# Kernel tuning notes

Hardware: AMD Instinct MI355X
Metric: run time of the kernel (lower is better)

## Reference

```python
import jax, jax.numpy as jnp
import numpy as np

HEAD_SIZE = 64
BLOCK_SIZE = 4096
BATCH = 4


def setup_inputs() -> dict:
    key = jax.random.key(0)
    kx, kk, kq, kv = jax.random.split(key, 4)
    x = jax.random.normal(kx, (BATCH, BLOCK_SIZE, HEAD_SIZE), dtype=jnp.float32)
    s = HEAD_SIZE ** -0.5  # ~ torch default linear init scale
    Wk = jax.random.uniform(kk, (HEAD_SIZE, HEAD_SIZE), jnp.float32, -s, s)
    Wq = jax.random.uniform(kq, (HEAD_SIZE, HEAD_SIZE), jnp.float32, -s, s)
    Wv = jax.random.uniform(kv, (HEAD_SIZE, HEAD_SIZE), jnp.float32, -s, s)
    return {"x": x, "Wk": Wk, "Wq": Wq, "Wv": Wv}


def reference(x, Wk, Wq, Wv):
    # x: [B, T, C]; W*: [C, C] stored torch-style (out, in) -> y = x @ W.T
    B, T, C = x.shape
    k = x @ Wk.T  # [B, T, C]
    q = x @ Wq.T
    v = x @ Wv.T
    scores = jnp.einsum('btc,bsc->bts', q, k) * (C ** -0.5)  # [B, T, T]
    causal = jnp.tril(jnp.ones((T, T), dtype=bool))
    scores = jnp.where(causal, scores, -jnp.inf)
    weights = jax.nn.softmax(scores, axis=-1)
    out = jnp.einsum('bts,bsc->btc', weights, v)  # [B, T, C]
    return out
```

## Files before the change

kernel.cpp:

```cpp
#include <hip/hip_runtime.h>
#include <hip/hip_bf16.h>

typedef unsigned short u16;
typedef unsigned int u32;
typedef __bf16 bf16x8_t __attribute__((ext_vector_type(8)));
typedef float f32x4_t __attribute__((ext_vector_type(4)));

constexpr int Bb = 4;
constexpr int Tt = 4096;
constexpr int Dd = 64;
constexpr float QSCALE = 0.18033688011112042f;

__device__ __forceinline__ u16 f2bf(float f) {
  unsigned int u = __builtin_bit_cast(unsigned int, f);
  return (u16)((u + 0x7fffu + ((u >> 16) & 1u)) >> 16);
}
__device__ __forceinline__ u32 pk2(float a, float b) {
  return (u32)f2bf(a) | ((u32)f2bf(b) << 16);
}
__device__ __forceinline__ u32 pkt(float a, float b) {
  const u32 ua = __builtin_bit_cast(u32, a);
  const u32 ub = __builtin_bit_cast(u32, b);
  return (ua >> 16) | (ub & 0xFFFF0000u);
}
__device__ __forceinline__ bf16x8_t ld16(const u16* p) {
  int4 v = *(const int4*)p;
  return __builtin_bit_cast(bf16x8_t, v);
}
__device__ __forceinline__ bf16x8_t cvtld8(const float* p) {
  float4 a = ((const float4*)p)[0];
  float4 b = ((const float4*)p)[1];
  union { u32 u[4]; bf16x8_t v; } r;
  r.u[0] = pk2(a.x, a.y); r.u[1] = pk2(a.z, a.w);
  r.u[2] = pk2(b.x, b.y); r.u[3] = pk2(b.z, b.w);
  return r.v;
}
__device__ __forceinline__ f32x4_t mfma16(bf16x8_t a, bf16x8_t b, f32x4_t c) {
  return __builtin_amdgcn_mfma_f32_16x16x32_bf16(a, b, c, 0, 0, 0);
}

__global__ __launch_bounds__(256) void HeadV1_proj(
    const float* __restrict__ x, const float* __restrict__ Wk,
    const float* __restrict__ Wq, const float* __restrict__ Wv,
    u16* __restrict__ qS, u16* __restrict__ kS, u16* __restrict__ vS)
{
  __shared__ u16 ylds[64][72];

  const int t = threadIdx.x;
  const int w = t >> 6, lane = t & 63, l15 = lane & 15, quad = lane >> 4;
  const int r0 = blockIdx.x * 64;
  const int b  = r0 >> 12;
  const int kt = (r0 & 4095) >> 6;
  const long tilebase = ((long)(b * 64 + kt)) * 4096;

  bf16x8_t xf[2];
  #pragma unroll
  for (int kh = 0; kh < 2; kh++)
    xf[kh] = cvtld8(x + (long)(r0 + w * 16 + l15) * 64 + kh * 32 + quad * 8);

  const float* Ws[3] = {Wk, Wq, Wv};
  u16* dsts[3];
  dsts[0] = kS + tilebase; dsts[1] = qS + tilebase; dsts[2] = vS + tilebase;

  #pragma unroll
  for (int m = 0; m < 3; m++) {
    float vals[4][4];
    #pragma unroll
    for (int g = 0; g < 4; g++) {
      f32x4_t acc = {0.f, 0.f, 0.f, 0.f};
      #pragma unroll
      for (int kh = 0; kh < 2; kh++) {
        bf16x8_t wf = cvtld8(Ws[m] + (g * 16 + l15) * 64 + kh * 32 + quad * 8);
        acc = mfma16(xf[kh], wf, acc);
      }
      #pragma unroll
      for (int r = 0; r < 4; r++)
        vals[g][r] = (m == 1) ? acc[r] * QSCALE : acc[r];
    }
    #pragma unroll
    for (int g = 0; g < 4; g++)
      #pragma unroll
      for (int r = 0; r < 4; r++)
        ylds[w * 16 + quad * 4 + r][g * 16 + l15] = f2bf(vals[g][r]);
    __syncthreads();
    if (m < 2) {
      #pragma unroll
      for (int kk = 0; kk < 2; kk++) {
        bf16x8_t f = ld16(&ylds[w * 16 + l15][kk * 32 + quad * 8]);
        *(int4*)(dsts[m] + (w * 2 + kk) * 512 + lane * 8) = __builtin_bit_cast(int4, f);
      }
    } else {
      #pragma unroll
      for (int kk = 0; kk < 2; kk++) {
        u16 tmp[8];
        #pragma unroll
        for (int j = 0; j < 8; j++)
          tmp[j] = ylds[kk * 32 + quad * 8 + j][w * 16 + l15];
        *(int4*)(dsts[2] + (kk * 4 + w) * 512 + lane * 8) = *(const int4*)tmp;
      }
    }
    __syncthreads();
  }
}

__global__ __launch_bounds__(512, 2) void HeadV1_flash(
    const u16* __restrict__ qS, const u16* __restrict__ kS,
    const u16* __restrict__ vS, float* __restrict__ outg)
{
  __shared__ __align__(16) char smem[56320];
  u16  (*pT)[32][72]   = (u16 (*)[32][72])smem;
  float (*chk)[16][68] = (float (*)[16][68])smem;
  float (*stg)[68]     = (float (*)[68])(smem + 36864);
  float (*lst)[64]     = (float (*)[64])(smem + 54272);

  const int t    = threadIdx.x;
  const int w    = t >> 6;
  const int lane = t & 63;
  const int l15  = lane & 15;
  const int quad = lane >> 4;

  const int b  = blockIdx.x & 3;
  const int qt = 63 - (blockIdx.x >> 2);
  const int qr0 = qt * 64;
  const long base = (long)b * Tt * Dd;

  union { u32 u4[4]; bf16x8_t v; } uo;
  uo.u4[0] = uo.u4[1] = uo.u4[2] = uo.u4[3] = 0x3F803F80u;
  const bf16x8_t ones = uo.v;
  const f32x4_t zero4 = {0.f, 0.f, 0.f, 0.f};

  const u16* qtile = qS + ((long)(b * 64 + qt)) * 4096 + lane * 8;
  bf16x8_t qfrag[4][2];
  #pragma unroll
  for (int ct = 0; ct < 4; ct++)
    #pragma unroll
    for (int kk = 0; kk < 2; kk++)
      qfrag[ct][kk] = ld16(qtile + (ct * 2 + kk) * 512);

  f32x4_t O[4][4];
  #pragma unroll
  for (int a = 0; a < 4; a++)
    #pragma unroll
    for (int c = 0; c < 4; c++)
      O[a][c] = zero4;
  f32x4_t Lc[4] = {zero4, zero4, zero4, zero4};

  const int nk = qt + 1;

  for (int kt = w; kt < nk; kt += 8) {
    const bool ismask = (kt == qt);
    const u16* ktile = kS + ((long)(b * 64 + kt)) * 4096 + lane * 8;
    const u16* vtile = vS + ((long)(b * 64 + kt)) * 4096 + lane * 8;

    bf16x8_t kfrag[4][2];
    #pragma unroll
    for (int rt = 0; rt < 4; rt++)
      #pragma unroll
      for (int kk = 0; kk < 2; kk++)
        kfrag[rt][kk] = ld16(ktile + (rt * 2 + kk) * 512);
    bf16x8_t vf[2][4];
    #pragma unroll
    for (int kk = 0; kk < 2; kk++)
      #pragma unroll
      for (int dt = 0; dt < 4; dt++)
        vf[kk][dt] = ld16(vtile + (kk * 4 + dt) * 512);

    #pragma unroll
    for (int half = 0; half < 2; half++) {
      #pragma unroll
      for (int rt = 0; rt < 4; rt++) {
        f32x4_t acc[2];
        #pragma unroll
        for (int cl = 0; cl < 2; cl++) {
          const int ct = half * 2 + cl;
          f32x4_t a = zero4;
          a = mfma16(kfrag[rt][0], qfrag[ct][0], a);
          a = mfma16(kfrag[rt][1], qfrag[ct][1], a);
          acc[cl] = a;
        }
        if (ismask) {
          const int kvl = rt * 16 + quad * 4;
          #pragma unroll
          for (int cl = 0; cl < 2; cl++) {
            const int ql = half * 32 + cl * 16 + l15;
            #pragma unroll
            for (int r = 0; r < 4; r++)
              if (kvl + r > ql) acc[cl][r] = -1e30f;
          }
        }
        #pragma unroll
        for (int cl = 0; cl < 2; cl++) {
          const float p0 = __builtin_amdgcn_exp2f(acc[cl][0]);
          const float p1 = __builtin_amdgcn_exp2f(acc[cl][1]);
          const float p2 = __builtin_amdgcn_exp2f(acc[cl][2]);
          const float p3 = __builtin_amdgcn_exp2f(acc[cl][3]);
          uint2 pk;
          pk.x = pkt(p0, p1);
          pk.y = pkt(p2, p3);
          *(uint2*)&pT[w][cl * 16 + l15][rt * 16 + quad * 4] = pk;
        }
      }
      #pragma unroll
      for (int kk = 0; kk < 2; kk++) {
        bf16x8_t pf0 = ld16(&pT[w][l15][kk * 32 + quad * 8]);
        bf16x8_t pf1 = ld16(&pT[w][16 + l15][kk * 32 + quad * 8]);
        #pragma unroll
        for (int dt = 0; dt < 4; dt++) {
          O[dt][half * 2]     = mfma16(vf[kk][dt], pf0, O[dt][half * 2]);
          O[dt][half * 2 + 1] = mfma16(vf[kk][dt], pf1, O[dt][half * 2 + 1]);
        }
        Lc[half * 2]     = mfma16(ones, pf0, Lc[half * 2]);
        Lc[half * 2 + 1] = mfma16(ones, pf1, Lc[half * 2 + 1]);
      }
    }
  }

  if (quad == 0) {
    #pragma unroll
    for (int ct = 0; ct < 4; ct++)
      lst[w][ct * 16 + l15] = Lc[ct][0];
  }
  __syncthreads();

  #pragma unroll
  for (int dt = 0; dt < 4; dt++) {
    #pragma unroll
    for (int ct = 0; ct < 4; ct++)
      #pragma unroll
      for (int r = 0; r < 4; r++)
        chk[w][quad * 4 + r][ct * 16 + l15] = O[dt][ct][r];
    __syncthreads();
    #pragma unroll
    for (int h = 0; h < 2; h++) {
      const int pos = t + h * 512;
      const int d2 = pos >> 6, q = pos & 63;
      float s = 0.f;
      #pragma unroll
      for (int w2 = 0; w2 < 8; w2++) s += chk[w2][d2][q];
      stg[q][dt * 16 + d2] = s;
    }
    __syncthreads();
  }

  {
    const int q = t >> 3, d0 = (t & 7) * 8;
    float L = 0.f;
    #pragma unroll
    for (int w2 = 0; w2 < 8; w2++) L += lst[w2][q];
    const float invL = 1.0f / L;
    float ov[8];
    #pragma unroll
    for (int i = 0; i < 8; i++) ov[i] = stg[q][d0 + i] * invL;
    float* dst = outg + base + (long)(qr0 + q) * 64 + d0;
    *(float4*)dst       = *(const float4*)&ov[0];
    *(float4*)(dst + 4) = *(const float4*)&ov[4];
  }
}

extern "C" void kernel_launch(void* const* d_in, const int* in_sizes, int n_in,
                              void* d_out, int out_size, void* d_ws, size_t ws_size,
                              hipStream_t stream) {
  (void)in_sizes; (void)n_in; (void)out_size; (void)ws_size;
  const float* x  = (const float*)d_in[0];
  const float* Wk = (const float*)d_in[1];
  const float* Wq = (const float*)d_in[2];
  const float* Wv = (const float*)d_in[3];
  float* out = (float*)d_out;
  u16* qw  = (u16*)d_ws;
  u16* kw  = qw + (size_t)Bb * Tt * Dd;
  u16* vw  = kw + (size_t)Bb * Tt * Dd;

  HeadV1_proj<<<(Bb * Tt) / 64, 256, 0, stream>>>(x, Wk, Wq, Wv, qw, kw, vw);
  HeadV1_flash<<<256, 512, 0, stream>>>(qw, kw, vw, out);
}
```

Before: 90.53 us.

## Prefetch next K/V tile into registers and relax launch bounds occupancy

Each wave now loads the K and V fragments for its next key tile into registers while computing on the current tile, double-buffering global loads to hide memory latency. The launch bounds minimum blocks per CU drops from 2 to 1, which lets the compiler use more registers for the extra buffers. The cost is roughly double the fragment register footprint and possibly lower occupancy, which reduces latency hiding across waves. A loop variable is also renamed in the reduction epilogue.

```diff
diff --git a/kernel.cpp b/kernel.cpp
--- a/kernel.cpp
+++ b/kernel.cpp
@@ -103,7 +103,7 @@
   }
 }
 
-__global__ __launch_bounds__(512, 2) void HeadV1_flash(
+__global__ __launch_bounds__(512, 1) void HeadV1_flash(
     const u16* __restrict__ qS, const u16* __restrict__ kS,
     const u16* __restrict__ vS, float* __restrict__ outg)
 {
@@ -147,23 +147,42 @@
 
   const int nk = qt + 1;
 
+  bf16x8_t kcur[4][2], vcur[2][4];
+  if (w < nk) {
+    const u16* kt0 = kS + ((long)(b * 64 + w)) * 4096 + lane * 8;
+    const u16* vt0 = vS + ((long)(b * 64 + w)) * 4096 + lane * 8;
+    #pragma unroll
+    for (int rt = 0; rt < 4; rt++)
+      #pragma unroll
+      for (int kk = 0; kk < 2; kk++)
+        kcur[rt][kk] = ld16(kt0 + (rt * 2 + kk) * 512);
+    #pragma unroll
+    for (int kk = 0; kk < 2; kk++)
+      #pragma unroll
+      for (int dt = 0; dt < 4; dt++)
+        vcur[kk][dt] = ld16(vt0 + (kk * 4 + dt) * 512);
+  }
+
   for (int kt = w; kt < nk; kt += 8) {
     const bool ismask = (kt == qt);
-    const u16* ktile = kS + ((long)(b * 64 + kt)) * 4096 + lane * 8;
-    const u16* vtile = vS + ((long)(b * 64 + kt)) * 4096 + lane * 8;
-
-    bf16x8_t kfrag[4][2];
-    #pragma unroll
-    for (int rt = 0; rt < 4; rt++)
+
+    const int ktn = kt + 8;
+    const bool havenext = (ktn < nk);
+    bf16x8_t knxt[4][2], vnxt[2][4];
+    if (havenext) {
+      const u16* ktile2 = kS + ((long)(b * 64 + ktn)) * 4096 + lane * 8;
+      const u16* vtile2 = vS + ((long)(b * 64 + ktn)) * 4096 + lane * 8;
+      #pragma unroll
+      for (int rt = 0; rt < 4; rt++)
+        #pragma unroll
+        for (int kk = 0; kk < 2; kk++)
+          knxt[rt][kk] = ld16(ktile2 + (rt * 2 + kk) * 512);
       #pragma unroll
       for (int kk = 0; kk < 2; kk++)
-        kfrag[rt][kk] = ld16(ktile + (rt * 2 + kk) * 512);
-    bf16x8_t vf[2][4];
-    #pragma unroll
-    for (int kk = 0; kk < 2; kk++)
-      #pragma unroll
-      for (int dt = 0; dt < 4; dt++)
-        vf[kk][dt] = ld16(vtile + (kk * 4 + dt) * 512);
+        #pragma unroll
+        for (int dt = 0; dt < 4; dt++)
+          vnxt[kk][dt] = ld16(vtile2 + (kk * 4 + dt) * 512);
+    }
 
     #pragma unroll
     for (int half = 0; half < 2; half++) {
@@ -174,8 +193,8 @@
         for (int cl = 0; cl < 2; cl++) {
           const int ct = half * 2 + cl;
           f32x4_t a = zero4;
-          a = mfma16(kfrag[rt][0], qfrag[ct][0], a);
-          a = mfma16(kfrag[rt][1], qfrag[ct][1], a);
+          a = mfma16(kcur[rt][0], qfrag[ct][0], a);
+          a = mfma16(kcur[rt][1], qfrag[ct][1], a);
           acc[cl] = a;
         }
         if (ismask) {
@@ -206,13 +225,26 @@
         bf16x8_t pf1 = ld16(&pT[w][16 + l15][kk * 32 + quad * 8]);
         #pragma unroll
         for (int dt = 0; dt < 4; dt++) {
-          O[dt][half * 2]     = mfma16(vf[kk][dt], pf0, O[dt][half * 2]);
-          O[dt][half * 2 + 1] = mfma16(vf[kk][dt], pf1, O[dt][half * 2 + 1]);
+          O[dt][half * 2]     = mfma16(vcur[kk][dt], pf0, O[dt][half * 2]);
+          O[dt][half * 2 + 1] = mfma16(vcur[kk][dt], pf1, O[dt][half * 2 + 1]);
         }
         Lc[half * 2]     = mfma16(ones, pf0, Lc[half * 2]);
         Lc[half * 2 + 1] = mfma16(ones, pf1, Lc[half * 2 + 1]);
       }
     }
+
+    if (havenext) {
+      #pragma unroll
+      for (int rt = 0; rt < 4; rt++)
+        #pragma unroll
+        for (int kk = 0; kk < 2; kk++)
+          kcur[rt][kk] = knxt[rt][kk];
+      #pragma unroll
+      for (int kk = 0; kk < 2; kk++)
+        #pragma unroll
+        for (int dt = 0; dt < 4; dt++)
+          vcur[kk][dt] = vnxt[kk][dt];
+    }
   }
 
   if (quad == 0) {
@@ -231,8 +263,8 @@
         chk[w][quad * 4 + r][ct * 16 + l15] = O[dt][ct][r];
     __syncthreads();
     #pragma unroll
-    for (int h = 0; h < 2; h++) {
-      const int pos = t + h * 512;
+    for (int hh = 0; hh < 2; hh++) {
+      const int pos = t + hh * 512;
       const int d2 = pos >> 6, q = pos & 63;
       float s = 0.f;
       #pragma unroll
```

Result: slower. 99.97 us (+10.4%).

## Halve flash query tile to 32 rows and pair heavy/light blocks

Applied to the files above, without the earlier changes.

The flash kernel now processes 32 query rows per block instead of 64, doubling the grid to 512 blocks. Block indices are remapped so the first and second halves walk the causal triangle in opposite directions, which evens out work across CUs. Shared memory and registers shrink, and launch bounds rise to allow 4 blocks per CU for better occupancy. K/V tiles are now loaded twice as often in total, and the 64-wide K tile is only half-used on the diagonal.

```diff
diff --git a/kernel.cpp b/kernel.cpp
--- a/kernel.cpp
+++ b/kernel.cpp
@@ -103,15 +103,15 @@
   }
 }
 
-__global__ __launch_bounds__(512, 2) void HeadV1_flash(
+__global__ __launch_bounds__(512, 4) void HeadV1_flash(
     const u16* __restrict__ qS, const u16* __restrict__ kS,
     const u16* __restrict__ vS, float* __restrict__ outg)
 {
-  __shared__ __align__(16) char smem[56320];
-  u16  (*pT)[32][72]   = (u16 (*)[32][72])smem;
-  float (*chk)[16][68] = (float (*)[16][68])smem;
-  float (*stg)[68]     = (float (*)[68])(smem + 36864);
-  float (*lst)[64]     = (float (*)[64])(smem + 54272);
+  __shared__ __align__(16) char smem[26624];
+  u16  (*pT)[32][36]   = (u16 (*)[32][36])smem;
+  float (*chk)[16][33] = (float (*)[16][33])smem;
+  float (*stg)[68]     = (float (*)[68])(smem + 16896);
+  float (*lst)[32]     = (float (*)[32])(smem + 25600);
 
   const int t    = threadIdx.x;
   const int w    = t >> 6;
@@ -119,9 +119,12 @@
   const int l15  = lane & 15;
   const int quad = lane >> 4;
 
-  const int b  = blockIdx.x & 3;
-  const int qt = 63 - (blockIdx.x >> 2);
-  const int qr0 = qt * 64;
+  const int b = blockIdx.x & 3;
+  const int u = blockIdx.x >> 2;
+  const int j = (u < 64) ? u : (191 - u);
+  const int qt64 = j >> 1;
+  const int ql0  = (j & 1) * 32;
+  const int qr0  = j * 32;
   const long base = (long)b * Tt * Dd;
 
   union { u32 u4[4]; bf16x8_t v; } uo;
@@ -129,95 +132,78 @@
   const bf16x8_t ones = uo.v;
   const f32x4_t zero4 = {0.f, 0.f, 0.f, 0.f};
 
-  const u16* qtile = qS + ((long)(b * 64 + qt)) * 4096 + lane * 8;
-  bf16x8_t qfrag[4][2];
-  #pragma unroll
-  for (int ct = 0; ct < 4; ct++)
-    #pragma unroll
-    for (int kk = 0; kk < 2; kk++)
-      qfrag[ct][kk] = ld16(qtile + (ct * 2 + kk) * 512);
-
-  f32x4_t O[4][4];
+  const u16* qtile = qS + ((long)(b * 64 + qt64)) * 4096 + lane * 8;
+  bf16x8_t qfrag[2][2];
+  #pragma unroll
+  for (int ct = 0; ct < 2; ct++)
+    #pragma unroll
+    for (int kd = 0; kd < 2; kd++)
+      qfrag[ct][kd] = ld16(qtile + ((ql0 / 16 + ct) * 2 + kd) * 512);
+
+  f32x4_t O[4][2];
   #pragma unroll
   for (int a = 0; a < 4; a++)
     #pragma unroll
-    for (int c = 0; c < 4; c++)
+    for (int c = 0; c < 2; c++)
       O[a][c] = zero4;
-  f32x4_t Lc[4] = {zero4, zero4, zero4, zero4};
-
-  const int nk = qt + 1;
+  f32x4_t Lc[2] = {zero4, zero4};
+
+  const int nk = (j >> 1) + 1;
 
   for (int kt = w; kt < nk; kt += 8) {
-    const bool ismask = (kt == qt);
+    const bool ismask = (kt == nk - 1);
+    const int kv0 = kt * 64;
     const u16* ktile = kS + ((long)(b * 64 + kt)) * 4096 + lane * 8;
     const u16* vtile = vS + ((long)(b * 64 + kt)) * 4096 + lane * 8;
 
-    bf16x8_t kfrag[4][2];
-    #pragma unroll
-    for (int rt = 0; rt < 4; rt++)
-      #pragma unroll
-      for (int kk = 0; kk < 2; kk++)
-        kfrag[rt][kk] = ld16(ktile + (rt * 2 + kk) * 512);
-    bf16x8_t vf[2][4];
-    #pragma unroll
-    for (int kk = 0; kk < 2; kk++)
+    #pragma unroll
+    for (int kk = 0; kk < 2; kk++) {
+      bf16x8_t vf[4];
       #pragma unroll
       for (int dt = 0; dt < 4; dt++)
-        vf[kk][dt] = ld16(vtile + (kk * 4 + dt) * 512);
-
-    #pragma unroll
-    for (int half = 0; half < 2; half++) {
-      #pragma unroll
-      for (int rt = 0; rt < 4; rt++) {
-        f32x4_t acc[2];
+        vf[dt] = ld16(vtile + (kk * 4 + dt) * 512);
+
+      #pragma unroll
+      for (int rtl = 0; rtl < 2; rtl++) {
+        const int rt = kk * 2 + rtl;
+        bf16x8_t kf0 = ld16(ktile + (rt * 2 + 0) * 512);
+        bf16x8_t kf1 = ld16(ktile + (rt * 2 + 1) * 512);
         #pragma unroll
-        for (int cl = 0; cl < 2; cl++) {
-          const int ct = half * 2 + cl;
-          f32x4_t a = zero4;
-          a = mfma16(kfrag[rt][0], qfrag[ct][0], a);
-          a = mfma16(kfrag[rt][1], qfrag[ct][1], a);
-          acc[cl] = a;
-        }
-        if (ismask) {
-          const int kvl = rt * 16 + quad * 4;
-          #pragma unroll
-          for (int cl = 0; cl < 2; cl++) {
-            const int ql = half * 32 + cl * 16 + l15;
+        for (int ct = 0; ct < 2; ct++) {
+          f32x4_t acc = zero4;
+          acc = mfma16(kf0, qfrag[ct][0], acc);
+          acc = mfma16(kf1, qfrag[ct][1], acc);
+          if (ismask) {
+            const int kvl = kv0 + rt * 16 + quad * 4;
+            const int qi  = qr0 + ct * 16 + l15;
             #pragma unroll
             for (int r = 0; r < 4; r++)
-              if (kvl + r > ql) acc[cl][r] = -1e30f;
+              if (kvl + r > qi) acc[r] = -1e30f;
           }
-        }
-        #pragma unroll
-        for (int cl = 0; cl < 2; cl++) {
-          const float p0 = __builtin_amdgcn_exp2f(acc[cl][0]);
-          const float p1 = __builtin_amdgcn_exp2f(acc[cl][1]);
-          const float p2 = __builtin_amdgcn_exp2f(acc[cl][2]);
-          const float p3 = __builtin_amdgcn_exp2f(acc[cl][3]);
+          const float p0 = __builtin_amdgcn_exp2f(acc[0]);
+          const float p1 = __builtin_amdgcn_exp2f(acc[1]);
+          const float p2 = __builtin_amdgcn_exp2f(acc[2]);
+          const float p3 = __builtin_amdgcn_exp2f(acc[3]);
           uint2 pk;
           pk.x = pkt(p0, p1);
           pk.y = pkt(p2, p3);
-          *(uint2*)&pT[w][cl * 16 + l15][rt * 16 + quad * 4] = pk;
+          *(uint2*)&pT[w][ct * 16 + l15][rtl * 16 + quad * 4] = pk;
         }
       }
       #pragma unroll
-      for (int kk = 0; kk < 2; kk++) {
-        bf16x8_t pf0 = ld16(&pT[w][l15][kk * 32 + quad * 8]);
-        bf16x8_t pf1 = ld16(&pT[w][16 + l15][kk * 32 + quad * 8]);
+      for (int ct = 0; ct < 2; ct++) {
+        bf16x8_t pf = ld16(&pT[w][ct * 16 + l15][quad * 8]);
         #pragma unroll
-        for (int dt = 0; dt < 4; dt++) {
-          O[dt][half * 2]     = mfma16(vf[kk][dt], pf0, O[dt][half * 2]);
-          O[dt][half * 2 + 1] = mfma16(vf[kk][dt], pf1, O[dt][half * 2 + 1]);
-        }
-        Lc[half * 2]     = mfma16(ones, pf0, Lc[half * 2]);
-        Lc[half * 2 + 1] = mfma16(ones, pf1, Lc[half * 2 + 1]);
+        for (int dt = 0; dt < 4; dt++)
+          O[dt][ct] = mfma16(vf[dt], pf, O[dt][ct]);
+        Lc[ct] = mfma16(ones, pf, Lc[ct]);
       }
     }
   }
 
   if (quad == 0) {
     #pragma unroll
-    for (int ct = 0; ct < 4; ct++)
+    for (int ct = 0; ct < 2; ct++)
       lst[w][ct * 16 + l15] = Lc[ct][0];
   }
   __syncthreads();
@@ -225,15 +211,13 @@
   #pragma unroll
   for (int dt = 0; dt < 4; dt++) {
     #pragma unroll
-    for (int ct = 0; ct < 4; ct++)
+    for (int ct = 0; ct < 2; ct++)
       #pragma unroll
       for (int r = 0; r < 4; r++)
         chk[w][quad * 4 + r][ct * 16 + l15] = O[dt][ct][r];
     __syncthreads();
-    #pragma unroll
-    for (int h = 0; h < 2; h++) {
-      const int pos = t + h * 512;
-      const int d2 = pos >> 6, q = pos & 63;
+    {
+      const int d2 = t >> 5, q = t & 31;
       float s = 0.f;
       #pragma unroll
       for (int w2 = 0; w2 < 8; w2++) s += chk[w2][d2][q];
@@ -243,17 +227,14 @@
   }
 
   {
-    const int q = t >> 3, d0 = (t & 7) * 8;
+    const int q = t >> 4, dg = t & 15;
     float L = 0.f;
     #pragma unroll
     for (int w2 = 0; w2 < 8; w2++) L += lst[w2][q];
     const float invL = 1.0f / L;
-    float ov[8];
-    #pragma unroll
-    for (int i = 0; i < 8; i++) ov[i] = stg[q][d0 + i] * invL;
-    float* dst = outg + base + (long)(qr0 + q) * 64 + d0;
-    *(float4*)dst       = *(const float4*)&ov[0];
-    *(float4*)(dst + 4) = *(const float4*)&ov[4];
+    float4 v = *(const float4*)&stg[q][dg * 4];
+    v.x *= invL; v.y *= invL; v.z *= invL; v.w *= invL;
+    *(float4*)(outg + base + (long)(qr0 + q) * 64 + dg * 4) = v;
   }
 }
 
@@ -271,5 +252,5 @@
   u16* vw  = kw + (size_t)Bb * Tt * Dd;
 
   HeadV1_proj<<<(Bb * Tt) / 64, 256, 0, stream>>>(x, Wk, Wq, Wv, qw, kw, vw);
-  HeadV1_flash<<<256, 512, 0, stream>>>(qw, kw, vw, out);
-}
+  HeadV1_flash<<<512, 512, 0, stream>>>(qw, kw, vw, out);
+}
```

After: 89.96 us. Within noise of the previous version (-0.6%).
